# Performance work log

Measured on AMD Instinct MI355X. Metric: run time of the kernel, lower is better.

The kernel has to match this reference:

```python
import jax, jax.numpy as jnp
import numpy as np

N = 50000      # num_nodes
E = 800000     # num_edges (avg degree 16)
D = 128        # input_dim = hidden_dim = output_dim
L = 3          # num_layers
EPS = 1e-5     # BatchNorm eps


def setup_inputs() -> dict:
    key = jax.random.key(0)
    k_x, k_e, k_w, k_b = jax.random.split(key, 4)
    x = jax.random.normal(k_x, (N, D), dtype=jnp.float32)
    edge_index = jax.random.randint(k_e, (2, E), 0, N, dtype=jnp.int32)
    # Stacked per-layer params: GCN weight/bias + BatchNorm gamma/beta
    Ws = jax.random.normal(k_w, (L, D, D), dtype=jnp.float32) * (1.0 / np.sqrt(D))
    bs = jax.random.normal(k_b, (L, D), dtype=jnp.float32) * 0.01
    gammas = jnp.ones((L, D), dtype=jnp.float32)
    betas = jnp.zeros((L, D), dtype=jnp.float32)
    return {"x": x, "edge_index": edge_index, "Ws": Ws, "bs": bs,
            "gammas": gammas, "betas": betas}


def reference(x, edge_index, Ws, bs, gammas, betas):
    """CausalGNN forward: L x (GCNConv -> BN(train stats) -> ReLU[not last]) with residuals.
    Dropout p=0 (deterministic). GCNConv is PyG-style: add self-loops, symmetric
    D^{-1/2} (A+I) D^{-1/2} normalization, linear transform + bias."""
    src, dst = edge_index[0], edge_index[1]
    # degree including self-loop (+1), computed at aggregation index
    deg = jax.ops.segment_sum(jnp.ones((E,), jnp.float32), dst, num_segments=N) + 1.0
    dis = jax.lax.rsqrt(deg)                       # deg >= 1, safe
    norm = dis[src] * dis[dst]                      # [E] edge norm
    self_norm = dis * dis                           # [N] self-loop norm = 1/deg

    for i in range(L):
        h = x @ Ws[i]                               # [N, D]
        # scatter-add aggregation of normalized neighbor messages
        agg = jax.ops.segment_sum(h[src] * norm[:, None], dst, num_segments=N)
        agg = agg + self_norm[:, None] * h + bs[i]
        # BatchNorm1d (training mode: biased batch statistics over nodes)
        mean = jnp.mean(agg, axis=0)
        var = jnp.mean(jnp.square(agg - mean), axis=0)
        y = gammas[i] * (agg - mean) * jax.lax.rsqrt(var + EPS) + betas[i]
        if i < L - 1:
            y = jax.nn.relu(y)
        x = x + y if i > 0 else y                   # residual (dims match)
    return x
```

## Files before the change

### kernel.cpp

```cpp
#include <hip/hip_runtime.h>
#include <hip/hip_bf16.h>
#include <hip/hip_fp16.h>

#define N_ 50000
#define E_ 800000
#define D_ 128
#define L_ 3

#define GG 782
#define NB 391
#define BCAP 3072
#define PB 200
#define PE 4000

typedef _Float16 half8 __attribute__((ext_vector_type(8)));
typedef float f32x4 __attribute__((ext_vector_type(4)));


__device__ inline float4 hcvt(uint2 u) {
    __half2 h0 = *(__half2*)&u.x;
    __half2 h1 = *(__half2*)&u.y;
    float2 f0 = __half22float2(h0);
    float2 f1 = __half22float2(h1);
    return make_float4(f0.x, f0.y, f1.x, f1.y);
}

__device__ inline unsigned pkh(float a, float b) {
    __half2 h = __floats2half2_rn(a, b);
    return *(unsigned*)&h;
}

__device__ inline unsigned short pkh1(float a) {
    _Float16 h = (_Float16)a;
    return *(unsigned short*)&h;
}


__global__ __launch_bounds__(256) void k_part(const int* __restrict__ src,
                                              const int* __restrict__ dst,
                                              const float* __restrict__ Ws,
                                              unsigned short* __restrict__ Wb,
                                              int* __restrict__ bucket_cnt,
                                              unsigned int* __restrict__ binned) {
    int b = blockIdx.x;
    if (b >= PB) {
        int l = b - PB;
        const float* Wl = Ws + l * 16384;
        unsigned short* Wo = Wb + l * 16384;
        for (int i = threadIdx.x; i < 16384; i += 256) {
            int n = i >> 7, k = i & 127;
            Wo[n * 128 + k] = pkh1(Wl[k * 128 + n]);
        }
        return;
    }
    __shared__ int hcnt[NB];
    __shared__ int hbase[NB];
    int t = threadIdx.x;
    for (int i = t; i < NB; i += 256) hcnt[i] = 0;
    __syncthreads();
    int e0 = b * PE;
    int dreg[16], sreg[16], oreg[16];
#pragma unroll
    for (int it = 0; it < 16; ++it) {
        int i = t + it * 256;
        if (i < PE) {
            int e = e0 + i;
            int d = dst[e];
            dreg[it] = d;
            sreg[it] = src[e];
            oreg[it] = atomicAdd(&hcnt[d >> 7], 1);
        }
    }
    __syncthreads();
    for (int i = t; i < NB; i += 256) {
        int c = hcnt[i];
        hbase[i] = c ? atomicAdd(&bucket_cnt[i], c) : 0;
    }
    __syncthreads();
#pragma unroll
    for (int it = 0; it < 16; ++it) {
        int i = t + it * 256;
        if (i < PE) {
            int d = dreg[it];
            int bk = d >> 7;
            binned[bk * BCAP + hbase[bk] + oreg[it]] =
                ((unsigned)(d & 127) << 16) | (unsigned)sreg[it];
        }
    }
}


__global__ __launch_bounds__(512) void k_bscan(const int* __restrict__ bucket_cnt,
                                               int* __restrict__ bucket_base,
                                               int* __restrict__ row_ptr) {
    __shared__ int wsum[8];
    int t = threadIdx.x;
    int lane = t & 63, wid = t >> 6;
    int v = (t < NB) ? bucket_cnt[t] : 0;
    int inc = v;
#pragma unroll
    for (int o = 1; o < 64; o <<= 1) {
        int u = __shfl_up(inc, o);
        if (lane >= o) inc += u;
    }
    if (lane == 63) wsum[wid] = inc;
    __syncthreads();
    if (wid == 0) {
        int w = (lane < 8) ? wsum[lane] : 0;
#pragma unroll
        for (int o = 1; o < 8; o <<= 1) {
            int u = __shfl_up(w, o);
            if (lane >= o) w += u;
        }
        if (lane < 8) wsum[lane] = w;
    }
    __syncthreads();
    int woff = wid ? wsum[wid - 1] : 0;
    if (t < NB) bucket_base[t] = inc + woff - v;
    if (t == 0) row_ptr[N_] = E_;
}


__device__ __forceinline__ void bin_body(const unsigned int* __restrict__ binned,
                                         const int* __restrict__ bucket_cnt,
                                         const int* __restrict__ bucket_base,
                                         int* __restrict__ row_ptr,
                                         float* __restrict__ dis,
                                         int* __restrict__ csr_src, int b) {
    __shared__ int h[128];
    __shared__ int hs[128];
    __shared__ int wtot[2];
    int t = threadIdx.x;
    if (t < 128) h[t] = 0;
    __syncthreads();
    int cnt  = bucket_cnt[b];
    int base = bucket_base[b];
    const unsigned int* bp = binned + b * BCAP;
    unsigned int pk[12];
    int off[12];
#pragma unroll
    for (int it = 0; it < 12; ++it) {
        int i = t + it * 256;
        if (i < cnt) {
            unsigned int p = bp[i];
            pk[it] = p;
            off[it] = atomicAdd(&h[p >> 16], 1);
        }
    }
    __syncthreads();
    int v = (t < 128) ? h[t] : 0;
    int lane = t & 63, wid = t >> 6;
    int inc = v;
#pragma unroll
    for (int o = 1; o < 64; o <<= 1) {
        int u = __shfl_up(inc, o);
        if (lane >= o) inc += u;
    }
    if (lane == 63 && wid < 2) wtot[wid] = inc;
    __syncthreads();
    if (wid == 1) inc += wtot[0];
    if (t < 128) {
        hs[t] = inc - v;
        int node = b * 128 + t;
        if (node < N_) {
            dis[node] = rsqrtf((float)v + 1.0f);
            row_ptr[node] = base + (inc - v);
        }
    }
    __syncthreads();
#pragma unroll
    for (int it = 0; it < 12; ++it) {
        int i = t + it * 256;
        if (i < cnt) {
            unsigned int p = pk[it];
            csr_src[base + hs[p >> 16] + off[it]] = (int)(p & 0xFFFFu);
        }
    }
}


template <bool IN16>
__device__ __forceinline__ void gemm_body(const void* __restrict__ Xin,
                                          const unsigned short* __restrict__ Wb,
                                          const float* __restrict__ disp,
                                          uint4* __restrict__ Hb,
                                          const float* __restrict__ st,
                                          const float* __restrict__ gamma,
                                          const float* __restrict__ beta,
                                          const unsigned short* __restrict__ resH,
                                          unsigned short* __restrict__ xoutH,
                                          int blk) {
    __shared__ unsigned short wt[128 * 136];
    __shared__ unsigned short xb[64 * 136];
    __shared__ float sab[256];
    int t  = threadIdx.x;
    int r0 = blk * 64;

    if (st) {
        if (t < 128) {
            float s = 0.f, s2 = 0.f;
#pragma unroll
            for (int k = 0; k < 8; ++k) {
                s  += st[k * 256 + t];
                s2 += st[k * 256 + 128 + t];
            }
            float mean = s * (1.0f / N_);
            float var  = s2 * (1.0f / N_) - mean * mean;
            float a = gamma[t] * rsqrtf(var + 1e-5f);
            sab[t]       = a;
            sab[128 + t] = beta[t] - mean * a;
        }
        __syncthreads();
    }

#pragma unroll
    for (int j = 0; j < 8; ++j) {
        int i = t + 256 * j;
        int row = i >> 4, c16 = i & 15;
        *(uint4*)&wt[row * 136 + c16 * 8] = ((const uint4*)Wb)[i];
    }
#pragma unroll
    for (int j = 0; j < 8; ++j) {
        int g   = t + 256 * j;
        int row = g >> 5;
        int c4  = (g & 31) * 4;
        int gr  = r0 + row;
        float4 v = make_float4(0.f, 0.f, 0.f, 0.f);
        if (gr < N_) {
            if constexpr (IN16) {
                v = hcvt(*(const uint2*)((const unsigned short*)Xin + gr * 128 + c4));
            } else {
                v = *(const float4*)((const float*)Xin + gr * 128 + c4);
            }
            if (st) {
                v.x = fmaxf(sab[c4] * v.x + sab[128 + c4], 0.f);
                v.y = fmaxf(sab[c4 + 1] * v.y + sab[128 + c4 + 1], 0.f);
                v.z = fmaxf(sab[c4 + 2] * v.z + sab[128 + c4 + 2], 0.f);
                v.w = fmaxf(sab[c4 + 3] * v.w + sab[128 + c4 + 3], 0.f);
                if (resH) {
                    float4 rr = hcvt(*(const uint2*)(resH + gr * 128 + c4));
                    v.x += rr.x; v.y += rr.y; v.z += rr.z; v.w += rr.w;
                }
            }
        }
        uint2 p;
        p.x = pkh(v.x, v.y);
        p.y = pkh(v.z, v.w);
        if (st && gr < N_) *(uint2*)(xoutH + gr * 128 + c4) = p;
        *(uint2*)&xb[row * 136 + c4] = p;
    }
    __syncthreads();

    int wv   = t >> 6;
    int lane = t & 63;
    int ln   = lane & 15;
    int quad = lane >> 4;

    const unsigned short* arow = &xb[(wv * 16 + ln) * 136 + quad * 8];
    half8 af[4];
#pragma unroll
    for (int ks = 0; ks < 4; ++ks) af[ks] = *(const half8*)(arow + ks * 32);

    f32x4 acc[8];
#pragma unroll
    for (int ct = 0; ct < 8; ++ct) acc[ct] = (f32x4){0.f, 0.f, 0.f, 0.f};

#pragma unroll
    for (int ct = 0; ct < 8; ++ct) {
        const unsigned short* wp = &wt[(ct * 16 + ln) * 136 + quad * 8];
#pragma unroll
        for (int ks = 0; ks < 4; ++ks) {
            half8 bf = *(const half8*)(wp + ks * 32);
            acc[ct] = __builtin_amdgcn_mfma_f32_16x16x32_f16(af[ks], bf, acc[ct], 0, 0, 0);
        }
    }

    float dr[4] = {1.f, 1.f, 1.f, 1.f};
    if (disp) {
#pragma unroll
        for (int reg = 0; reg < 4; ++reg) {
            int r = r0 + wv * 16 + quad * 4 + reg;
            dr[reg] = disp[r < N_ ? r : (N_ - 1)];
        }
    }
    __syncthreads();
#pragma unroll
    for (int ct = 0; ct < 8; ++ct) {
#pragma unroll
        for (int reg = 0; reg < 4; ++reg) {
            int lrow = wv * 16 + quad * 4 + reg;
            xb[lrow * 136 + ct * 16 + ln] = pkh1(acc[ct][reg] * dr[reg]);
        }
    }
    __syncthreads();
#pragma unroll
    for (int j = 0; j < 4; ++j) {
        int i = t + 256 * j;
        int row = i >> 4, c16 = i & 15;
        int gr = r0 + row;
        if (gr < N_) Hb[gr * 16 + c16] = *(uint4*)&xb[row * 136 + c16 * 8];
    }
}


__global__ __launch_bounds__(256) void k_fillg(const unsigned int* __restrict__ binned,
                                               const int* __restrict__ bucket_cnt,
                                               const int* __restrict__ bucket_base,
                                               int* __restrict__ row_ptr,
                                               float* __restrict__ dis,
                                               int* __restrict__ csr_src,
                                               const float* __restrict__ x,
                                               const unsigned short* __restrict__ Wb,
                                               uint4* __restrict__ Hb) {
    int b = blockIdx.x;
    if (b < NB) {
        bin_body(binned, bucket_cnt, bucket_base, row_ptr, dis, csr_src, b);
    } else {
        gemm_body<false>(x, Wb, nullptr, Hb, nullptr, nullptr, nullptr, nullptr,
                         nullptr, b - NB);
    }
}


__global__ __launch_bounds__(256) void k_gemm(const unsigned short* __restrict__ Xin,
                                              const unsigned short* __restrict__ Wb,
                                              const float* __restrict__ disp,
                                              uint4* __restrict__ Hb,
                                              const float* __restrict__ st,
                                              const float* __restrict__ gamma,
                                              const float* __restrict__ beta,
                                              const unsigned short* __restrict__ resH,
                                              unsigned short* __restrict__ xoutH) {
    gemm_body<true>(Xin, Wb, disp, Hb, st, gamma, beta, resH, xoutH, blockIdx.x);
}


template <bool SCALED, bool OUT16>
__global__ __launch_bounds__(256) void k_agg(const uint4* __restrict__ Hb,
                                             const int* __restrict__ row_ptr,
                                             const int* __restrict__ csr_src,
                                             const float* __restrict__ dis,
                                             const float* __restrict__ bias,
                                             void* __restrict__ AGGout,
                                             float* __restrict__ stats2) {
    int tid  = threadIdx.x;
    int sub  = tid >> 4;
    int lane = tid & 15;
    int node = blockIdx.x * 16 + sub;

    int beg = row_ptr[node], end = row_ptr[node + 1];
    float dn = dis[node];
    uint4 su = Hb[node * 16 + lane];
    float4 f0s = hcvt(make_uint2(su.x, su.y));
    float4 f1s = hcvt(make_uint2(su.z, su.w));
    float4 acc0, acc1;
    if constexpr (SCALED) {
        acc0 = f0s; acc1 = f1s;
    } else {
        acc0.x = dn * f0s.x; acc0.y = dn * f0s.y; acc0.z = dn * f0s.z; acc0.w = dn * f0s.w;
        acc1.x = dn * f1s.x; acc1.y = dn * f1s.y; acc1.z = dn * f1s.z; acc1.w = dn * f1s.w;
    }

    for (int c = beg; c < end; c += 16) {
        int m = end - c; if (m > 16) m = 16;
        int idx = 0; float dsv = 0.f;
        if (lane < m) {
            idx = csr_src[c + lane];
            if constexpr (!SCALED) dsv = dis[idx];
        }
        int j = 0;
        for (; j + 8 <= m; j += 8) {
            int s[8]; float d[8]; uint4 a[8];
#pragma unroll
            for (int k = 0; k < 8; ++k) {
                s[k] = __shfl(idx, j + k, 16);
                if constexpr (!SCALED) d[k] = __shfl(dsv, j + k, 16);
            }
#pragma unroll
            for (int k = 0; k < 8; ++k) a[k] = Hb[s[k] * 16 + lane];
#pragma unroll
            for (int k = 0; k < 8; ++k) {
                float4 f0 = hcvt(make_uint2(a[k].x, a[k].y));
                float4 f1 = hcvt(make_uint2(a[k].z, a[k].w));
                if constexpr (SCALED) {
                    acc0.x += f0.x; acc0.y += f0.y; acc0.z += f0.z; acc0.w += f0.w;
                    acc1.x += f1.x; acc1.y += f1.y; acc1.z += f1.z; acc1.w += f1.w;
                } else {
                    acc0.x += d[k] * f0.x; acc0.y += d[k] * f0.y;
                    acc0.z += d[k] * f0.z; acc0.w += d[k] * f0.w;
                    acc1.x += d[k] * f1.x; acc1.y += d[k] * f1.y;
                    acc1.z += d[k] * f1.z; acc1.w += d[k] * f1.w;
                }
            }
        }
        for (; j + 4 <= m; j += 4) {
            int s[4]; float d[4]; uint4 a[4];
#pragma unroll
            for (int k = 0; k < 4; ++k) {
                s[k] = __shfl(idx, j + k, 16);
                if constexpr (!SCALED) d[k] = __shfl(dsv, j + k, 16);
            }
#pragma unroll
            for (int k = 0; k < 4; ++k) a[k] = Hb[s[k] * 16 + lane];
#pragma unroll
            for (int k = 0; k < 4; ++k) {
                float4 f0 = hcvt(make_uint2(a[k].x, a[k].y));
                float4 f1 = hcvt(make_uint2(a[k].z, a[k].w));
                if constexpr (SCALED) {
                    acc0.x += f0.x; acc0.y += f0.y; acc0.z += f0.z; acc0.w += f0.w;
                    acc1.x += f1.x; acc1.y += f1.y; acc1.z += f1.z; acc1.w += f1.w;
                } else {
                    acc0.x += d[k] * f0.x; acc0.y += d[k] * f0.y;
                    acc0.z += d[k] * f0.z; acc0.w += d[k] * f0.w;
                    acc1.x += d[k] * f1.x; acc1.y += d[k] * f1.y;
                    acc1.z += d[k] * f1.z; acc1.w += d[k] * f1.w;
                }
            }
        }
        for (; j < m; ++j) {
            int s0 = __shfl(idx, j, 16);
            float d0 = 0.f;
            if constexpr (!SCALED) d0 = __shfl(dsv, j, 16);
            uint4 a0 = Hb[s0 * 16 + lane];
            float4 f0 = hcvt(make_uint2(a0.x, a0.y));
            float4 f1 = hcvt(make_uint2(a0.z, a0.w));
            if constexpr (SCALED) {
                acc0.x += f0.x; acc0.y += f0.y; acc0.z += f0.z; acc0.w += f0.w;
                acc1.x += f1.x; acc1.y += f1.y; acc1.z += f1.z; acc1.w += f1.w;
            } else {
                acc0.x += d0 * f0.x; acc0.y += d0 * f0.y;
                acc0.z += d0 * f0.z; acc0.w += d0 * f0.w;
                acc1.x += d0 * f1.x; acc1.y += d0 * f1.y;
                acc1.z += d0 * f1.z; acc1.w += d0 * f1.w;
            }
        }
    }

    float4 b0 = *(const float4*)(bias + lane * 8);
    float4 b1 = *(const float4*)(bias + lane * 8 + 4);
    float4 r0, r1;
    r0.x = dn * acc0.x + b0.x; r0.y = dn * acc0.y + b0.y;
    r0.z = dn * acc0.z + b0.z; r0.w = dn * acc0.w + b0.w;
    r1.x = dn * acc1.x + b1.x; r1.y = dn * acc1.y + b1.y;
    r1.z = dn * acc1.z + b1.z; r1.w = dn * acc1.w + b1.w;

    if constexpr (OUT16) {
        uint4 p;
        p.x = pkh(r0.x, r0.y); p.y = pkh(r0.z, r0.w);
        p.z = pkh(r1.x, r1.y); p.w = pkh(r1.z, r1.w);
        ((uint4*)AGGout)[node * 16 + lane] = p;
    } else {
        ((float4*)AGGout)[node * 32 + lane * 2]     = r0;
        ((float4*)AGGout)[node * 32 + lane * 2 + 1] = r1;
    }

    __shared__ float sbuf[16][128];
    float4* sp = (float4*)&sbuf[sub][lane * 8];
    sp[0] = r0; sp[1] = r1;
    __syncthreads();
    if (tid < 128) {
        float s = 0.f, s2 = 0.f;
#pragma unroll
        for (int k = 0; k < 16; ++k) {
            float v = sbuf[k][tid];
            s += v; s2 += v * v;
        }
        float* stp = stats2 + (blockIdx.x & 7) * 256;
        atomicAdd(&stp[tid], s);
        atomicAdd(&stp[128 + tid], s2);
    }
}


__global__ __launch_bounds__(256) void k_normF(const float4* __restrict__ AGG,
                                               const unsigned short* __restrict__ resH,
                                               const float* __restrict__ st,
                                               const float* __restrict__ gamma,
                                               const float* __restrict__ beta,
                                               float4* __restrict__ OUT) {
    __shared__ float sab[256];
    int t = threadIdx.x;
    if (t < 128) {
        float s = 0.f, s2 = 0.f;
#pragma unroll
        for (int k = 0; k < 8; ++k) {
            s  += st[k * 256 + t];
            s2 += st[k * 256 + 128 + t];
        }
        float mean = s * (1.0f / N_);
        float var  = s2 * (1.0f / N_) - mean * mean;
        float a = gamma[t] * rsqrtf(var + 1e-5f);
        sab[t]       = a;
        sab[128 + t] = beta[t] - mean * a;
    }
    __syncthreads();
    for (int i = blockIdx.x * 256 + t; i < N_ * 32; i += gridDim.x * 256) {
        int f4 = (i & 31) * 4;
        float4 v = AGG[i];
        float4 rr = hcvt(((const uint2*)resH)[i]);
        v.x = sab[f4] * v.x + sab[128 + f4] + rr.x;
        v.y = sab[f4 + 1] * v.y + sab[128 + f4 + 1] + rr.y;
        v.z = sab[f4 + 2] * v.z + sab[128 + f4 + 2] + rr.z;
        v.w = sab[f4 + 3] * v.w + sab[128 + f4 + 3] + rr.w;
        OUT[i] = v;
    }
}


extern "C" void kernel_launch(void* const* d_in, const int* in_sizes, int n_in,
                              void* d_out, int out_size, void* d_ws, size_t ws_size,
                              hipStream_t stream) {
    const float* x      = (const float*)d_in[0];
    const int*   ei     = (const int*)d_in[1];
    const float* Ws     = (const float*)d_in[2];
    const float* bs     = (const float*)d_in[3];
    const float* gammas = (const float*)d_in[4];
    const float* betas  = (const float*)d_in[5];
    float* out = (float*)d_out;

    const int* src = ei;
    const int* dst = ei + E_;

    char* w = (char*)d_ws;
    float* stats2      = (float*)(w + 0);
    int*   bucket_cnt  = (int*)(w + 24576);
    int*   bucket_base = (int*)(w + 26144);
    int*   row_ptr     = (int*)(w + 27712);
    float* dis         = (float*)(w + 227728);
    int*   csr_src     = (int*)(w + 427728);
    uint4* Hb          = (uint4*)(w + 3627776);
    unsigned short* XBh = (unsigned short*)(w + 16427776);
    unsigned short* Wb  = (unsigned short*)(w + 29227776);

    unsigned short* AGG16 = (unsigned short*)out;
    float* AGG = out;

    unsigned int* binned = (unsigned int*)XBh;

    hipMemsetAsync(d_ws, 0, 26144, stream);

    k_part<<<PB + 3, 256, 0, stream>>>(src, dst, Ws, Wb, bucket_cnt, binned);
    k_bscan<<<1, 512, 0, stream>>>(bucket_cnt, bucket_base, row_ptr);
    k_fillg<<<NB + GG, 256, 0, stream>>>(binned, bucket_cnt, bucket_base, row_ptr,
                                         dis, csr_src, x, Wb, Hb);

    k_agg<false, true><<<N_ / 16, 256, 0, stream>>>(Hb, row_ptr, csr_src, dis, bs,
                                                    AGG16, stats2);
    k_gemm<<<GG, 256, 0, stream>>>(AGG16, Wb + 16384, dis, Hb,
                                   stats2, gammas, betas, nullptr, XBh);
    k_agg<true, true><<<N_ / 16, 256, 0, stream>>>(Hb, row_ptr, csr_src, dis, bs + D_,
                                                   AGG16, stats2 + 2048);
    k_gemm<<<GG, 256, 0, stream>>>(AGG16, Wb + 32768, dis, Hb,
                                   stats2 + 2048, gammas + D_, betas + D_, XBh, XBh);
    k_agg<true, false><<<N_ / 16, 256, 0, stream>>>(Hb, row_ptr, csr_src, dis, bs + 2 * D_,
                                                    AGG, stats2 + 4096);
    k_normF<<<1024, 256, 0, stream>>>((const float4*)AGG, XBh,
                                      stats2 + 4096, gammas + 2 * D_, betas + 2 * D_,
                                      (float4*)out);
}
```

Before: 268.7 us.

## Fold bucket scan into bin kernel, prefetch CSR indices, fp32 intermediates with nontemporal stores

Removes the separate single-block bucket scan kernel; each bin block now computes its own base by summing the preceding bucket counts. The aggregation loop software-pipelines the next chunk of CSR source indices and degree scales with nontemporal loads. Intermediate aggregation outputs switch from fp16 to fp32 with nontemporal stores, and the final normalize kernel uses nontemporal loads and stores. This saves one launch and some index latency but doubles intermediate write and read traffic, and adds redundant prefix sums across bin blocks.

```diff
diff --git a/kernel.cpp b/kernel.cpp
--- a/kernel.cpp
+++ b/kernel.cpp
@@ -15,6 +15,7 @@
 
 typedef _Float16 half8 __attribute__((ext_vector_type(8)));
 typedef float f32x4 __attribute__((ext_vector_type(4)));
+typedef unsigned int u32x4 __attribute__((ext_vector_type(4)));
 
 
 __device__ inline float4 hcvt(uint2 u) {
@@ -33,6 +34,16 @@
 __device__ inline unsigned short pkh1(float a) {
     _Float16 h = (_Float16)a;
     return *(unsigned short*)&h;
+}
+
+__device__ inline void ntst4(float4* p, float4 v) {
+    f32x4 t = {v.x, v.y, v.z, v.w};
+    __builtin_nontemporal_store(t, (f32x4*)p);
+}
+
+__device__ inline float4 ntld4(const float4* p) {
+    f32x4 v = __builtin_nontemporal_load((const f32x4*)p);
+    return make_float4(v.x, v.y, v.z, v.w);
 }
 
 
@@ -90,51 +101,28 @@
 }
 
 
-__global__ __launch_bounds__(512) void k_bscan(const int* __restrict__ bucket_cnt,
-                                               int* __restrict__ bucket_base,
-                                               int* __restrict__ row_ptr) {
-    __shared__ int wsum[8];
-    int t = threadIdx.x;
-    int lane = t & 63, wid = t >> 6;
-    int v = (t < NB) ? bucket_cnt[t] : 0;
-    int inc = v;
-#pragma unroll
-    for (int o = 1; o < 64; o <<= 1) {
-        int u = __shfl_up(inc, o);
-        if (lane >= o) inc += u;
-    }
-    if (lane == 63) wsum[wid] = inc;
-    __syncthreads();
-    if (wid == 0) {
-        int w = (lane < 8) ? wsum[lane] : 0;
-#pragma unroll
-        for (int o = 1; o < 8; o <<= 1) {
-            int u = __shfl_up(w, o);
-            if (lane >= o) w += u;
-        }
-        if (lane < 8) wsum[lane] = w;
-    }
-    __syncthreads();
-    int woff = wid ? wsum[wid - 1] : 0;
-    if (t < NB) bucket_base[t] = inc + woff - v;
-    if (t == 0) row_ptr[N_] = E_;
-}
-
-
 __device__ __forceinline__ void bin_body(const unsigned int* __restrict__ binned,
                                          const int* __restrict__ bucket_cnt,
-                                         const int* __restrict__ bucket_base,
                                          int* __restrict__ row_ptr,
                                          float* __restrict__ dis,
                                          int* __restrict__ csr_src, int b) {
     __shared__ int h[128];
     __shared__ int hs[128];
-    __shared__ int wtot[2];
+    __shared__ int wtot[4];
     int t = threadIdx.x;
+    int lane = t & 63, wid = t >> 6;
+
+    int part = 0;
+    for (int i = t; i < b; i += 256) part += bucket_cnt[i];
+#pragma unroll
+    for (int o = 32; o > 0; o >>= 1) part += __shfl_down(part, o, 64);
+    if (lane == 0) wtot[wid] = part;
     if (t < 128) h[t] = 0;
     __syncthreads();
-    int cnt  = bucket_cnt[b];
-    int base = bucket_base[b];
+    int base = wtot[0] + wtot[1] + wtot[2] + wtot[3];
+    __syncthreads();
+
+    int cnt = bucket_cnt[b];
     const unsigned int* bp = binned + b * BCAP;
     unsigned int pk[12];
     int off[12];
@@ -149,7 +137,6 @@
     }
     __syncthreads();
     int v = (t < 128) ? h[t] : 0;
-    int lane = t & 63, wid = t >> 6;
     int inc = v;
 #pragma unroll
     for (int o = 1; o < 64; o <<= 1) {
@@ -167,6 +154,7 @@
             row_ptr[node] = base + (inc - v);
         }
     }
+    if (b == 0 && t == 0) row_ptr[N_] = E_;
     __syncthreads();
 #pragma unroll
     for (int it = 0; it < 12; ++it) {
@@ -179,8 +167,7 @@
 }
 
 
-template <bool IN16>
-__device__ __forceinline__ void gemm_body(const void* __restrict__ Xin,
+__device__ __forceinline__ void gemm_body(const float* __restrict__ Xin,
                                           const unsigned short* __restrict__ Wb,
                                           const float* __restrict__ disp,
                                           uint4* __restrict__ Hb,
@@ -227,11 +214,7 @@
         int gr  = r0 + row;
         float4 v = make_float4(0.f, 0.f, 0.f, 0.f);
         if (gr < N_) {
-            if constexpr (IN16) {
-                v = hcvt(*(const uint2*)((const unsigned short*)Xin + gr * 128 + c4));
-            } else {
-                v = *(const float4*)((const float*)Xin + gr * 128 + c4);
-            }
+            v = *(const float4*)(Xin + gr * 128 + c4);
             if (st) {
                 v.x = fmaxf(sab[c4] * v.x + sab[128 + c4], 0.f);
                 v.y = fmaxf(sab[c4 + 1] * v.y + sab[128 + c4 + 1], 0.f);
@@ -305,7 +288,6 @@
 
 __global__ __launch_bounds__(256) void k_fillg(const unsigned int* __restrict__ binned,
                                                const int* __restrict__ bucket_cnt,
-                                               const int* __restrict__ bucket_base,
                                                int* __restrict__ row_ptr,
                                                float* __restrict__ dis,
                                                int* __restrict__ csr_src,
@@ -314,15 +296,15 @@
                                                uint4* __restrict__ Hb) {
     int b = blockIdx.x;
     if (b < NB) {
-        bin_body(binned, bucket_cnt, bucket_base, row_ptr, dis, csr_src, b);
+        bin_body(binned, bucket_cnt, row_ptr, dis, csr_src, b);
     } else {
-        gemm_body<false>(x, Wb, nullptr, Hb, nullptr, nullptr, nullptr, nullptr,
-                         nullptr, b - NB);
-    }
-}
-
-
-__global__ __launch_bounds__(256) void k_gemm(const unsigned short* __restrict__ Xin,
+        gemm_body(x, Wb, nullptr, Hb, nullptr, nullptr, nullptr, nullptr,
+                  nullptr, b - NB);
+    }
+}
+
+
+__global__ __launch_bounds__(256) void k_gemm(const float* __restrict__ Xin,
                                               const unsigned short* __restrict__ Wb,
                                               const float* __restrict__ disp,
                                               uint4* __restrict__ Hb,
@@ -331,17 +313,17 @@
                                               const float* __restrict__ beta,
                                               const unsigned short* __restrict__ resH,
                                               unsigned short* __restrict__ xoutH) {
-    gemm_body<true>(Xin, Wb, disp, Hb, st, gamma, beta, resH, xoutH, blockIdx.x);
-}
-
-
-template <bool SCALED, bool OUT16>
+    gemm_body(Xin, Wb, disp, Hb, st, gamma, beta, resH, xoutH, blockIdx.x);
+}
+
+
+template <bool SCALED>
 __global__ __launch_bounds__(256) void k_agg(const uint4* __restrict__ Hb,
                                              const int* __restrict__ row_ptr,
                                              const int* __restrict__ csr_src,
                                              const float* __restrict__ dis,
                                              const float* __restrict__ bias,
-                                             void* __restrict__ AGGout,
+                                             float4* __restrict__ AGG,
                                              float* __restrict__ stats2) {
     int tid  = threadIdx.x;
     int sub  = tid >> 4;
@@ -361,12 +343,22 @@
         acc1.x = dn * f1s.x; acc1.y = dn * f1s.y; acc1.z = dn * f1s.z; acc1.w = dn * f1s.w;
     }
 
-    for (int c = beg; c < end; c += 16) {
+    int c = beg;
+    int idx = 0; float dsv = 0.f;
+    {
+        int m0 = end - c; if (m0 > 16) m0 = 16;
+        if (lane < m0) {
+            idx = __builtin_nontemporal_load(csr_src + c + lane);
+            if constexpr (!SCALED) dsv = dis[idx];
+        }
+    }
+    while (c < end) {
         int m = end - c; if (m > 16) m = 16;
-        int idx = 0; float dsv = 0.f;
-        if (lane < m) {
-            idx = csr_src[c + lane];
-            if constexpr (!SCALED) dsv = dis[idx];
+        int nidx = 0; float ndsv = 0.f;
+        int nm = end - (c + 16); if (nm > 16) nm = 16;
+        if (lane < nm) {
+            nidx = __builtin_nontemporal_load(csr_src + c + 16 + lane);
+            if constexpr (!SCALED) ndsv = dis[nidx];
         }
         int j = 0;
         for (; j + 8 <= m; j += 8) {
@@ -419,7 +411,7 @@
         }
         for (; j < m; ++j) {
             int s0 = __shfl(idx, j, 16);
-            float d0 = 0.f;
+            float d0 = 1.f;
             if constexpr (!SCALED) d0 = __shfl(dsv, j, 16);
             uint4 a0 = Hb[s0 * 16 + lane];
             float4 f0 = hcvt(make_uint2(a0.x, a0.y));
@@ -434,6 +426,7 @@
                 acc1.z += d0 * f1.z; acc1.w += d0 * f1.w;
             }
         }
+        idx = nidx; dsv = ndsv; c += 16;
     }
 
     float4 b0 = *(const float4*)(bias + lane * 8);
@@ -443,16 +436,8 @@
     r0.z = dn * acc0.z + b0.z; r0.w = dn * acc0.w + b0.w;
     r1.x = dn * acc1.x + b1.x; r1.y = dn * acc1.y + b1.y;
     r1.z = dn * acc1.z + b1.z; r1.w = dn * acc1.w + b1.w;
-
-    if constexpr (OUT16) {
-        uint4 p;
-        p.x = pkh(r0.x, r0.y); p.y = pkh(r0.z, r0.w);
-        p.z = pkh(r1.x, r1.y); p.w = pkh(r1.z, r1.w);
-        ((uint4*)AGGout)[node * 16 + lane] = p;
-    } else {
-        ((float4*)AGGout)[node * 32 + lane * 2]     = r0;
-        ((float4*)AGGout)[node * 32 + lane * 2 + 1] = r1;
-    }
+    ntst4(&AGG[node * 32 + lane * 2], r0);
+    ntst4(&AGG[node * 32 + lane * 2 + 1], r1);
 
     __shared__ float sbuf[16][128];
     float4* sp = (float4*)&sbuf[sub][lane * 8];
@@ -496,13 +481,13 @@
     __syncthreads();
     for (int i = blockIdx.x * 256 + t; i < N_ * 32; i += gridDim.x * 256) {
         int f4 = (i & 31) * 4;
-        float4 v = AGG[i];
+        float4 v = ntld4(&AGG[i]);
         float4 rr = hcvt(((const uint2*)resH)[i]);
         v.x = sab[f4] * v.x + sab[128 + f4] + rr.x;
         v.y = sab[f4 + 1] * v.y + sab[128 + f4 + 1] + rr.y;
         v.z = sab[f4 + 2] * v.z + sab[128 + f4 + 2] + rr.z;
         v.w = sab[f4 + 3] * v.w + sab[128 + f4 + 3] + rr.w;
-        OUT[i] = v;
+        ntst4(&OUT[i], v);
     }
 }
 
@@ -524,15 +509,12 @@
     char* w = (char*)d_ws;
     float* stats2      = (float*)(w + 0);
     int*   bucket_cnt  = (int*)(w + 24576);
-    int*   bucket_base = (int*)(w + 26144);
     int*   row_ptr     = (int*)(w + 27712);
     float* dis         = (float*)(w + 227728);
     int*   csr_src     = (int*)(w + 427728);
     uint4* Hb          = (uint4*)(w + 3627776);
     unsigned short* XBh = (unsigned short*)(w + 16427776);
     unsigned short* Wb  = (unsigned short*)(w + 29227776);
-
-    unsigned short* AGG16 = (unsigned short*)out;
     float* AGG = out;
 
     unsigned int* binned = (unsigned int*)XBh;
@@ -540,20 +522,19 @@
     hipMemsetAsync(d_ws, 0, 26144, stream);
 
     k_part<<<PB + 3, 256, 0, stream>>>(src, dst, Ws, Wb, bucket_cnt, binned);
-    k_bscan<<<1, 512, 0, stream>>>(bucket_cnt, bucket_base, row_ptr);
-    k_fillg<<<NB + GG, 256, 0, stream>>>(binned, bucket_cnt, bucket_base, row_ptr,
+    k_fillg<<<NB + GG, 256, 0, stream>>>(binned, bucket_cnt, row_ptr,
                                          dis, csr_src, x, Wb, Hb);
 
-    k_agg<false, true><<<N_ / 16, 256, 0, stream>>>(Hb, row_ptr, csr_src, dis, bs,
-                                                    AGG16, stats2);
-    k_gemm<<<GG, 256, 0, stream>>>(AGG16, Wb + 16384, dis, Hb,
+    k_agg<false><<<N_ / 16, 256, 0, stream>>>(Hb, row_ptr, csr_src, dis, bs,
+                                              (float4*)AGG, stats2);
+    k_gemm<<<GG, 256, 0, stream>>>(AGG, Wb + 16384, dis, Hb,
                                    stats2, gammas, betas, nullptr, XBh);
-    k_agg<true, true><<<N_ / 16, 256, 0, stream>>>(Hb, row_ptr, csr_src, dis, bs + D_,
-                                                   AGG16, stats2 + 2048);
-    k_gemm<<<GG, 256, 0, stream>>>(AGG16, Wb + 32768, dis, Hb,
+    k_agg<true><<<N_ / 16, 256, 0, stream>>>(Hb, row_ptr, csr_src, dis, bs + D_,
+                                             (float4*)AGG, stats2 + 2048);
+    k_gemm<<<GG, 256, 0, stream>>>(AGG, Wb + 32768, dis, Hb,
                                    stats2 + 2048, gammas + D_, betas + D_, XBh, XBh);
-    k_agg<true, false><<<N_ / 16, 256, 0, stream>>>(Hb, row_ptr, csr_src, dis, bs + 2 * D_,
-                                                    AGG, stats2 + 4096);
+    k_agg<true><<<N_ / 16, 256, 0, stream>>>(Hb, row_ptr, csr_src, dis, bs + 2 * D_,
+                                             (float4*)AGG, stats2 + 4096);
     k_normF<<<1024, 256, 0, stream>>>((const float4*)AGG, XBh,
                                       stats2 + 4096, gammas + 2 * D_, betas + 2 * D_,
                                       (float4*)out);
```

Measured after the change: 265.6 us. About the same (-1.2%).
